# Kernel tuning notes

Measured on AMD Instinct MI355X. Metric: run time of the kernel, lower is better.

## Reference

```python
import jax, jax.numpy as jnp
import numpy as np

D_MODEL = 2048
NUM_HEADS = 16
HEAD_DIM = 128


def setup_inputs() -> dict:
    key = jax.random.key(0)
    ks = jax.random.split(key, 9)
    B, S = 2, 2048
    s_in = 1.0 / np.sqrt(D_MODEL)
    return {
        "x": jax.random.normal(ks[0], (B, S, D_MODEL), dtype=jnp.float32),
        "wq": jax.random.normal(ks[1], (D_MODEL, D_MODEL), dtype=jnp.float32) * s_in,
        "bq": jnp.zeros((D_MODEL,), jnp.float32),
        "wk": jax.random.normal(ks[2], (D_MODEL, HEAD_DIM), dtype=jnp.float32) * s_in,
        "bk": jnp.zeros((HEAD_DIM,), jnp.float32),
        "wv": jax.random.normal(ks[3], (D_MODEL, HEAD_DIM), dtype=jnp.float32) * s_in,
        "bv": jnpp_zeros(ks) if False else jnp.zeros((HEAD_DIM,), jnp.float32),
        "wo": jax.random.normal(ks[4], (D_MODEL, D_MODEL), dtype=jnp.float32) * s_in,
        "bo": jnp.zeros((D_MODEL,), jnp.float32),
    }


def reference(x, wq, bq, wk, bk, wv, bv, wo, bo):
    B, S, _ = x.shape
    H, Dh = NUM_HEADS, HEAD_DIM
    q = (x @ wq + bq).reshape(B, S, H, Dh)          # [B,S,H,Dh]
    k = x @ wk + bk                                  # [B,S,Dh] (single KV head)
    v = x @ wv + bv                                  # [B,S,Dh]
    scale = 1.0 / jnp.sqrt(jnp.asarray(Dh, x.dtype))
    # scores: [B,H,Sq,Sk] — MQA: K shared across heads
    scores = jnp.einsum('bqhd,bkd->bhqk', q, k) * scale
    attn = jax.nn.softmax(scores, axis=-1)
    out = jnp.einsum('bhqk,bkd->bqhd', attn, v).reshape(B, S, H * Dh)
    return out @ wo + bo
```

## Files before the change

kernel.cpp:

```cpp
#include <hip/hip_runtime.h>
#include <stdint.h>

typedef unsigned short u16;

#define D_MODEL 2048
#define HEADS 16
#define HDIM 128
#define SEQ 2048
#define BATCH 2
#define NROWS (BATCH*SEQ)
#define QKV_N (D_MODEL + 2*HDIM)

typedef __attribute__((ext_vector_type(8))) short bf16x8;
typedef __attribute__((ext_vector_type(4))) float f32x4;

__device__ inline u16 f2bf(float f) {
  union { float f; uint32_t u; } v; v.f = f;
  uint32_t r = v.u + 0x7FFFu + ((v.u >> 16) & 1u);
  return (u16)(r >> 16);
}
__device__ inline u16 f2bf_fast(float f) {
  union { float f; uint32_t u; } v; v.f = f;
  return (u16)((v.u + 0x8000u) >> 16);
}

__device__ inline void gload_lds16(const void* g, void* l) {
  __builtin_amdgcn_global_load_lds(
      (const __attribute__((address_space(1))) unsigned int*)g,
      (__attribute__((address_space(3))) unsigned int*)l, 16, 0, 0);
}

__global__ void cvt_bias(const float* __restrict__ s, u16* __restrict__ d,
                         const float* __restrict__ bq, const float* __restrict__ bk,
                         const float* __restrict__ bv, float* __restrict__ biasq) {
  const int bid = blockIdx.x;
  if (bid < 8192) {
    int i = bid * 256 + threadIdx.x;
    float4 f = ((const float4*)s)[i];
    ushort4 u;
    u.x = f2bf(f.x); u.y = f2bf(f.y); u.z = f2bf(f.z); u.w = f2bf(f.w);
    ((ushort4*)d)[i] = u;
  } else {
    for (int i = threadIdx.x; i < QKV_N; i += 256)
      biasq[i] = (i < D_MODEL) ? bq[i]
               : ((i < D_MODEL + HDIM) ? bk[i - D_MODEL] : bv[i - D_MODEL - HDIM]);
  }
}

__global__ void transpose_all(const float* __restrict__ wq, const float* __restrict__ wk,
                              const float* __restrict__ wv, const float* __restrict__ wo,
                              u16* __restrict__ wqkvT, u16* __restrict__ woT) {
  __shared__ float t[32][33];
  const int n0v = blockIdx.x * 32, k0 = blockIdx.y * 32;
  const float* src; int N, n0, drow; u16* dst;
  if (n0v < 2048)      { src = wq; N = 2048; n0 = n0v;        dst = wqkvT; drow = n0v; }
  else if (n0v < 2176) { src = wk; N = 128;  n0 = n0v - 2048; dst = wqkvT; drow = n0v; }
  else if (n0v < 2304) { src = wv; N = 128;  n0 = n0v - 2176; dst = wqkvT; drow = n0v; }
  else                 { src = wo; N = 2048; n0 = n0v - 2304; dst = woT;   drow = n0v - 2304; }
  const int tx = threadIdx.x, ty = threadIdx.y;
#pragma unroll
  for (int i = 0; i < 4; i++)
    t[ty + 8*i][tx] = src[(size_t)(k0 + ty + 8*i) * N + n0 + tx];
  __syncthreads();
#pragma unroll
  for (int i = 0; i < 4; i++)
    dst[(size_t)(drow + ty + 8*i) * D_MODEL + k0 + tx] = f2bf(t[tx][ty + 8*i]);
}

#define BM 128
#define BN 128
#define BK 32

__global__ __launch_bounds__(256) void gemm_bt(
    const u16* __restrict__ A, const u16* __restrict__ BT,
    const float* __restrict__ bias,
    u16* __restrict__ Cb, float* __restrict__ Cf,
    u16* __restrict__ vT,
    int M, int Nld, int colOff, int tilesN, int K) {
  __shared__ __align__(16) u16 sA[2][BM * BK];
  __shared__ __align__(16) u16 sB[2][BN * BK];
  const int tid = threadIdx.x;
  const int wave = tid >> 6, lane = tid & 63;
  const int bm = blockIdx.x / tilesN, bn = blockIdx.x % tilesN;
  const int m0 = bm * BM, n0 = bn * BN;
  const int wm = (wave & 1) * 64, wn = (wave >> 1) * 64;
  const int l16 = lane & 15, kq = (lane >> 4) * 8;

  f32x4 acc[4][4] = {};
  const int srow = lane >> 2, scol = (lane & 3) * 8;

#define GDMA(i, buf)                                                           \
  {                                                                            \
    const int _k0 = (i) * BK;                                                  \
    _Pragma("unroll") for (int c = 0; c < 2; c++) {                            \
      const int chunk = wave * 2 + c;                                          \
      const int row = chunk * 16 + srow;                                       \
      gload_lds16(&A[(size_t)(m0 + row) * K + _k0 + scol],                     \
                  &sA[buf][chunk * 512]);                                      \
      gload_lds16(&BT[(size_t)(n0 + row) * K + _k0 + scol],                    \
                  &sB[buf][chunk * 512]);                                      \
    }                                                                          \
  }

  const int NI = K / BK;
  GDMA(0, 0);
  for (int i = 0; i < NI; i++) {
    const int cur = i & 1;
    __syncthreads();
    if (i + 1 < NI) GDMA(i + 1, cur ^ 1);
    bf16x8 af[4], bfr[4];
#pragma unroll
    for (int mb = 0; mb < 4; ++mb) af[mb]  = *(const bf16x8*)&sA[cur][(wm + mb*16 + l16) * BK + kq];
#pragma unroll
    for (int nb = 0; nb < 4; ++nb) bfr[nb] = *(const bf16x8*)&sB[cur][(wn + nb*16 + l16) * BK + kq];
#pragma unroll
    for (int mb = 0; mb < 4; ++mb)
#pragma unroll
      for (int nb = 0; nb < 4; ++nb)
        acc[mb][nb] = __builtin_amdgcn_mfma_f32_16x16x32_bf16(af[mb], bfr[nb], acc[mb][nb], 0, 0, 0);
  }
#undef GDMA

#pragma unroll
  for (int mb = 0; mb < 4; ++mb) {
#pragma unroll
    for (int nb = 0; nb < 4; ++nb) {
      const int gnL = n0 + wn + nb * 16 + l16;
      const int gn = colOff + gnL;
      const float bb = bias ? bias[gnL] : 0.0f;
#pragma unroll
      for (int r = 0; r < 4; ++r) {
        const int gm = m0 + wm + mb * 16 + (lane >> 4) * 4 + r;
        const float v = acc[mb][nb][r] + bb;
        if (Cf) {
          Cf[(size_t)gm * Nld + gn] = v;
        } else {
          const u16 u = f2bf(v);
          Cb[(size_t)gm * Nld + gn] = u;
          if (vT && gn >= D_MODEL + HDIM) {
            const int bi = gm >> 11, si = gm & 2047;
            vT[((size_t)bi * HDIM + (gn - D_MODEL - HDIM)) * SEQ + si] = u;
          }
        }
      }
    }
  }
}

__global__ __launch_bounds__(256) void mqa_attn(
    const u16* __restrict__ qkv, const u16* __restrict__ vT, u16* __restrict__ ctx) {
  __shared__ __align__(16) u16 sK[2][64 * 128];
  __shared__ __align__(16) u16 sV[128 * 64];
  __shared__ __align__(16) u16 sP[4][32 * 64];
  const int tid = threadIdx.x, wave = tid >> 6, lane = tid & 63;
  const int qt = blockIdx.x & 15;
  const int h  = (blockIdx.x >> 4) & 15;
  const int b  = blockIdx.x >> 8;
  const int bS = b * SEQ;
  const int q0 = qt * 128 + wave * 32;
  const int l16 = lane & 15, quad = lane >> 4;
  const int sw = l16 & 7;
  u16* myP = &sP[wave][0];

  bf16x8 qf[2][4];
#pragma unroll
  for (int mb = 0; mb < 2; mb++)
#pragma unroll
    for (int kc = 0; kc < 4; kc++)
      qf[mb][kc] = *(const bf16x8*)&qkv[(size_t)(bS + q0 + mb*16 + l16) * QKV_N
                                        + h*HDIM + kc*32 + quad*8];

  f32x4 o[2][8] = {};
  float lrow[2] = {0.f, 0.f};
  const float sc2 = 0.08838834764831845f * 1.4426950408889634f;

  const u16* Kbase = qkv + (size_t)bS * QKV_N + D_MODEL;
  const u16* Vbase = vT + (size_t)b * HDIM * SEQ;

  const int kRowIn = lane >> 4;
  const int kChS   = lane & 15;
  const int vRowIn = lane >> 3;
  const int vChL   = (lane & 7) ^ (lane >> 3);

#define DMA_K(t, dst)                                                          \
  {                                                                            \
    const int _sk = (t) * 64;                                                  \
    _Pragma("unroll") for (int j = 0; j < 4; j++) {                            \
      const int i = wave * 4 + j;                                              \
      const int krow = i * 4 + kRowIn;                                         \
      const int kcl = kChS ^ (krow & 15);                                      \
      gload_lds16(&Kbase[(size_t)(_sk + krow) * QKV_N + kcl * 8],              \
                  &(dst)[i * 512]);                                            \
    }                                                                          \
  }
#define DMA_V(t)                                                               \
  {                                                                            \
    const int _sk = (t) * 64;                                                  \
    _Pragma("unroll") for (int j = 0; j < 4; j++) {                            \
      const int i = wave * 4 + j;                                              \
      const int d = i * 8 + vRowIn;                                            \
      gload_lds16(&Vbase[(size_t)d * SEQ + _sk + vChL * 8], &sV[i * 512]);     \
    }                                                                          \
  }

  DMA_K(0, sK[0]);
  DMA_V(0);
  __syncthreads();

  const int T = SEQ / 64;
  for (int t = 0; t < T; ++t) {
    const int cur = t & 1;
    if (t + 1 < T) DMA_K(t + 1, sK[cur ^ 1]);

    f32x4 sc[2][4];
#pragma unroll
    for (int nb = 0; nb < 4; nb++) {
      bf16x8 kf[4];
#pragma unroll
      for (int kc = 0; kc < 4; kc++)
        kf[kc] = *(const bf16x8*)&sK[cur][(nb*16 + l16) * 128 + (((kc*4 + quad) ^ l16) * 8)];
#pragma unroll
      for (int mb = 0; mb < 2; mb++) {
        f32x4 a = {0.f, 0.f, 0.f, 0.f};
#pragma unroll
        for (int kc = 0; kc < 4; kc++)
          a = __builtin_amdgcn_mfma_f32_16x16x32_bf16(kf[kc], qf[mb][kc], a, 0, 0, 0);
        sc[mb][nb] = a;
      }
    }

#pragma unroll
    for (int mb = 0; mb < 2; mb++)
#pragma unroll
      for (int nb = 0; nb < 4; nb++) {
        float p0 = __builtin_amdgcn_exp2f(sc[mb][nb][0] * sc2);
        float p1 = __builtin_amdgcn_exp2f(sc[mb][nb][1] * sc2);
        float p2 = __builtin_amdgcn_exp2f(sc[mb][nb][2] * sc2);
        float p3 = __builtin_amdgcn_exp2f(sc[mb][nb][3] * sc2);
        lrow[mb] += (p0 + p1) + (p2 + p3);
        uint32_t lo = (uint32_t)f2bf_fast(p0) | ((uint32_t)f2bf_fast(p1) << 16);
        uint32_t hi = (uint32_t)f2bf_fast(p2) | ((uint32_t)f2bf_fast(p3) << 16);
        uint2 w; w.x = lo; w.y = hi;
        const int pr = (nb*2 + (quad >> 1)) ^ sw;
        *(uint2*)&myP[(mb*16 + l16) * 64 + pr * 8 + (quad & 1) * 4] = w;
      }

    __syncthreads();

    bf16x8 pf[2][2];
#pragma unroll
    for (int mb = 0; mb < 2; mb++)
#pragma unroll
      for (int kc = 0; kc < 2; kc++)
        pf[mb][kc] = *(const bf16x8*)&myP[(mb*16 + l16) * 64 + (((kc*4 + quad) ^ sw) * 8)];
#pragma unroll
    for (int nb = 0; nb < 8; nb++) {
      bf16x8 vf[2];
#pragma unroll
      for (int kc = 0; kc < 2; kc++)
        vf[kc] = *(const bf16x8*)&sV[(nb*16 + l16) * 64 + (((kc*4 + quad) ^ (l16 & 7)) * 8)];
#pragma unroll
      for (int mb = 0; mb < 2; mb++)
#pragma unroll
        for (int kc = 0; kc < 2; kc++)
          o[mb][nb] = __builtin_amdgcn_mfma_f32_16x16x32_bf16(pf[mb][kc], vf[kc], o[mb][nb], 0, 0, 0);
    }

    __syncthreads();
    if (t + 1 < T) DMA_V(t + 1);
  }

#pragma unroll
  for (int mb = 0; mb < 2; mb++) {
    lrow[mb] += __shfl_xor(lrow[mb], 16, 64);
    lrow[mb] += __shfl_xor(lrow[mb], 32, 64);
  }
  float invl[2][4];
#pragma unroll
  for (int mb = 0; mb < 2; mb++)
#pragma unroll
    for (int r = 0; r < 4; r++)
      invl[mb][r] = 1.0f / __shfl(lrow[mb], quad * 4 + r, 64);

#pragma unroll
  for (int mb = 0; mb < 2; mb++)
#pragma unroll
    for (int nb = 0; nb < 8; nb++)
#pragma unroll
      for (int r = 0; r < 4; r++) {
        const int gq = q0 + mb*16 + quad*4 + r;
        const int gd = h * HDIM + nb*16 + l16;
        ctx[(size_t)(bS + gq) * D_MODEL + gd] = f2bf(o[mb][nb][r] * invl[mb][r]);
      }
}

extern "C" void kernel_launch(void* const* d_in, const int* in_sizes, int n_in,
                              void* d_out, int out_size, void* d_ws, size_t ws_size,
                              hipStream_t stream) {
  const float* x  = (const float*)d_in[0];
  const float* wq = (const float*)d_in[1];
  const float* bq = (const float*)d_in[2];
  const float* wk = (const float*)d_in[3];
  const float* bk = (const float*)d_in[4];
  const float* wv = (const float*)d_in[5];
  const float* bv = (const float*)d_in[6];
  const float* wo = (const float*)d_in[7];
  const float* bo = (const float*)d_in[8];
  float* out = (float*)d_out;
  char* ws = (char*)d_ws;

  u16*   xb    = (u16*)(ws + 0);
  u16*   wqkvT = (u16*)(ws + 16777216);
  u16*   woT   = (u16*)(ws + 26214400);
  u16*   qkv   = (u16*)(ws + 34603008);
  u16*   vT    = (u16*)(ws + 53477376);
  u16*   ctx   = (u16*)(ws + 54525952);
  float* biasq = (float*)(ws + 71303168);

  cvt_bias<<<8193, 256, 0, stream>>>(x, xb, bq, bk, bv, biasq);
  transpose_all<<<dim3(136, 64), dim3(32, 8), 0, stream>>>(wq, wk, wv, wo, wqkvT, woT);

  gemm_bt<<<32 * 16, 256, 0, stream>>>(xb, wqkvT, biasq, qkv, nullptr, nullptr,
                                       NROWS, QKV_N, 0, 16, D_MODEL);
  gemm_bt<<<32 * 2, 256, 0, stream>>>(xb, wqkvT + (size_t)D_MODEL * D_MODEL,
                                      biasq + D_MODEL, qkv, nullptr, vT,
                                      NROWS, QKV_N, D_MODEL, 2, D_MODEL);
  mqa_attn<<<BATCH * HEADS * (SEQ / 128), 256, 0, stream>>>(qkv, vT, ctx);
  gemm_bt<<<32 * 16, 256, 0, stream>>>(ctx, woT, bo, nullptr, out, nullptr,
                                       NROWS, D_MODEL, 0, 16, D_MODEL);
}
```

Measured before the change: 350.8 us.

## Fuse prep kernels, merge QKV GEMMs, widen K tile with XOR-swizzled LDS

Merges the bf16 conversion, bias packing and weight transpose kernels into one launch. Also merges the two QKV GEMM launches into a single 18-column-tile grid. The GEMM K tile grows from 32 to 64, and LDS is XOR-swizzled to avoid bank conflicts on fragment reads. The QKV GEMM uses a single LDS buffer, probably to raise occupancy, at the cost of less load/compute overlap.

```diff
diff --git a/kernel.cpp b/kernel.cpp
--- a/kernel.cpp
+++ b/kernel.cpp
@@ -30,94 +30,110 @@
       (__attribute__((address_space(3))) unsigned int*)l, 16, 0, 0);
 }
 
-__global__ void cvt_bias(const float* __restrict__ s, u16* __restrict__ d,
+__global__ void prep_all(const float* __restrict__ x, u16* __restrict__ xb,
+                         const float* __restrict__ wq, const float* __restrict__ wk,
+                         const float* __restrict__ wv, const float* __restrict__ wo,
+                         u16* __restrict__ wqkvT, u16* __restrict__ woT,
                          const float* __restrict__ bq, const float* __restrict__ bk,
                          const float* __restrict__ bv, float* __restrict__ biasq) {
-  const int bid = blockIdx.x;
+  const int bid = blockIdx.x, tid = threadIdx.x;
   if (bid < 8192) {
-    int i = bid * 256 + threadIdx.x;
-    float4 f = ((const float4*)s)[i];
+    int i = bid * 256 + tid;
+    float4 f = ((const float4*)x)[i];
     ushort4 u;
     u.x = f2bf(f.x); u.y = f2bf(f.y); u.z = f2bf(f.z); u.w = f2bf(f.w);
-    ((ushort4*)d)[i] = u;
+    ((ushort4*)xb)[i] = u;
+  } else if (bid < 16896) {
+    __shared__ float t[32][33];
+    const int b2 = bid - 8192;
+    const int n0v = (b2 % 136) * 32, k0 = (b2 / 136) * 32;
+    const float* src; int N, n0, drow; u16* dst;
+    if (n0v < 2048)      { src = wq; N = 2048; n0 = n0v;        dst = wqkvT; drow = n0v; }
+    else if (n0v < 2176) { src = wk; N = 128;  n0 = n0v - 2048; dst = wqkvT; drow = n0v; }
+    else if (n0v < 2304) { src = wv; N = 128;  n0 = n0v - 2176; dst = wqkvT; drow = n0v; }
+    else                 { src = wo; N = 2048; n0 = n0v - 2304; dst = woT;   drow = n0v - 2304; }
+    const int tx = tid & 31, ty = tid >> 5;
+#pragma unroll
+    for (int i = 0; i < 4; i++)
+      t[ty + 8*i][tx] = src[(size_t)(k0 + ty + 8*i) * N + n0 + tx];
+    __syncthreads();
+#pragma unroll
+    for (int i = 0; i < 4; i++)
+      dst[(size_t)(drow + ty + 8*i) * D_MODEL + k0 + tx] = f2bf(t[tx][ty + 8*i]);
   } else {
-    for (int i = threadIdx.x; i < QKV_N; i += 256)
+    for (int i = tid; i < QKV_N; i += 256)
       biasq[i] = (i < D_MODEL) ? bq[i]
                : ((i < D_MODEL + HDIM) ? bk[i - D_MODEL] : bv[i - D_MODEL - HDIM]);
   }
 }
 
-__global__ void transpose_all(const float* __restrict__ wq, const float* __restrict__ wk,
-                              const float* __restrict__ wv, const float* __restrict__ wo,
-                              u16* __restrict__ wqkvT, u16* __restrict__ woT) {
-  __shared__ float t[32][33];
-  const int n0v = blockIdx.x * 32, k0 = blockIdx.y * 32;
-  const float* src; int N, n0, drow; u16* dst;
-  if (n0v < 2048)      { src = wq; N = 2048; n0 = n0v;        dst = wqkvT; drow = n0v; }
-  else if (n0v < 2176) { src = wk; N = 128;  n0 = n0v - 2048; dst = wqkvT; drow = n0v; }
-  else if (n0v < 2304) { src = wv; N = 128;  n0 = n0v - 2176; dst = wqkvT; drow = n0v; }
-  else                 { src = wo; N = 2048; n0 = n0v - 2304; dst = woT;   drow = n0v - 2304; }
-  const int tx = threadIdx.x, ty = threadIdx.y;
-#pragma unroll
-  for (int i = 0; i < 4; i++)
-    t[ty + 8*i][tx] = src[(size_t)(k0 + ty + 8*i) * N + n0 + tx];
-  __syncthreads();
-#pragma unroll
-  for (int i = 0; i < 4; i++)
-    dst[(size_t)(drow + ty + 8*i) * D_MODEL + k0 + tx] = f2bf(t[tx][ty + 8*i]);
-}
-
 #define BM 128
 #define BN 128
-#define BK 32
-
+#define BKK 64
+
+template <bool DB>
 __global__ __launch_bounds__(256) void gemm_bt(
     const u16* __restrict__ A, const u16* __restrict__ BT,
     const float* __restrict__ bias,
     u16* __restrict__ Cb, float* __restrict__ Cf,
     u16* __restrict__ vT,
-    int M, int Nld, int colOff, int tilesN, int K) {
-  __shared__ __align__(16) u16 sA[2][BM * BK];
-  __shared__ __align__(16) u16 sB[2][BN * BK];
+    int M, int N, int tilesN, int K) {
+  __shared__ __align__(16) u16 sA[DB ? 2 : 1][BM * BKK];
+  __shared__ __align__(16) u16 sB[DB ? 2 : 1][BN * BKK];
   const int tid = threadIdx.x;
   const int wave = tid >> 6, lane = tid & 63;
   const int bm = blockIdx.x / tilesN, bn = blockIdx.x % tilesN;
   const int m0 = bm * BM, n0 = bn * BN;
   const int wm = (wave & 1) * 64, wn = (wave >> 1) * 64;
-  const int l16 = lane & 15, kq = (lane >> 4) * 8;
+  const int l16 = lane & 15, quad = lane >> 4;
 
   f32x4 acc[4][4] = {};
-  const int srow = lane >> 2, scol = (lane & 3) * 8;
+
+  const int dRow = lane >> 3;
+  const int dCol = ((lane & 7) ^ (lane >> 3)) * 8;
 
 #define GDMA(i, buf)                                                           \
   {                                                                            \
-    const int _k0 = (i) * BK;                                                  \
-    _Pragma("unroll") for (int c = 0; c < 2; c++) {                            \
-      const int chunk = wave * 2 + c;                                          \
-      const int row = chunk * 16 + srow;                                       \
-      gload_lds16(&A[(size_t)(m0 + row) * K + _k0 + scol],                     \
-                  &sA[buf][chunk * 512]);                                      \
-      gload_lds16(&BT[(size_t)(n0 + row) * K + _k0 + scol],                    \
-                  &sB[buf][chunk * 512]);                                      \
+    const int _k0 = (i) * BKK;                                                 \
+    _Pragma("unroll") for (int c = 0; c < 4; c++) {                            \
+      const int op = wave * 4 + c;                                             \
+      const int row = op * 8 + dRow;                                           \
+      gload_lds16(&A[(size_t)(m0 + row) * K + _k0 + dCol], &sA[buf][op * 512]);\
+      gload_lds16(&BT[(size_t)(n0 + row) * K + _k0 + dCol], &sB[buf][op * 512]);\
     }                                                                          \
   }
 
-  const int NI = K / BK;
+  const int NI = K / BKK;
   GDMA(0, 0);
   for (int i = 0; i < NI; i++) {
-    const int cur = i & 1;
+    const int cur = DB ? (i & 1) : 0;
     __syncthreads();
-    if (i + 1 < NI) GDMA(i + 1, cur ^ 1);
-    bf16x8 af[4], bfr[4];
-#pragma unroll
-    for (int mb = 0; mb < 4; ++mb) af[mb]  = *(const bf16x8*)&sA[cur][(wm + mb*16 + l16) * BK + kq];
-#pragma unroll
-    for (int nb = 0; nb < 4; ++nb) bfr[nb] = *(const bf16x8*)&sB[cur][(wn + nb*16 + l16) * BK + kq];
-#pragma unroll
-    for (int mb = 0; mb < 4; ++mb)
-#pragma unroll
-      for (int nb = 0; nb < 4; ++nb)
-        acc[mb][nb] = __builtin_amdgcn_mfma_f32_16x16x32_bf16(af[mb], bfr[nb], acc[mb][nb], 0, 0, 0);
+    if (DB && i + 1 < NI) GDMA(i + 1, cur ^ 1);
+#pragma unroll
+    for (int kk2 = 0; kk2 < 2; kk2++) {
+      bf16x8 af[4], bfr[4];
+#pragma unroll
+      for (int mb = 0; mb < 4; ++mb) {
+        const int R = wm + mb * 16 + l16;
+        const int s = (kk2 * 4 + quad) ^ (l16 & 7);
+        af[mb] = *(const bf16x8*)&sA[cur][R * BKK + s * 8];
+      }
+#pragma unroll
+      for (int nb = 0; nb < 4; ++nb) {
+        const int R = wn + nb * 16 + l16;
+        const int s = (kk2 * 4 + quad) ^ (l16 & 7);
+        bfr[nb] = *(const bf16x8*)&sB[cur][R * BKK + s * 8];
+      }
+#pragma unroll
+      for (int mb = 0; mb < 4; ++mb)
+#pragma unroll
+        for (int nb = 0; nb < 4; ++nb)
+          acc[mb][nb] = __builtin_amdgcn_mfma_f32_16x16x32_bf16(af[mb], bfr[nb], acc[mb][nb], 0, 0, 0);
+    }
+    if (!DB) {
+      __syncthreads();
+      if (i + 1 < NI) GDMA(i + 1, 0);
+    }
   }
 #undef GDMA
 
@@ -125,18 +141,17 @@
   for (int mb = 0; mb < 4; ++mb) {
 #pragma unroll
     for (int nb = 0; nb < 4; ++nb) {
-      const int gnL = n0 + wn + nb * 16 + l16;
-      const int gn = colOff + gnL;
-      const float bb = bias ? bias[gnL] : 0.0f;
+      const int gn = n0 + wn + nb * 16 + l16;
+      const float bb = bias ? bias[gn] : 0.0f;
 #pragma unroll
       for (int r = 0; r < 4; ++r) {
-        const int gm = m0 + wm + mb * 16 + (lane >> 4) * 4 + r;
+        const int gm = m0 + wm + mb * 16 + quad * 4 + r;
         const float v = acc[mb][nb][r] + bb;
         if (Cf) {
-          Cf[(size_t)gm * Nld + gn] = v;
+          Cf[(size_t)gm * N + gn] = v;
         } else {
           const u16 u = f2bf(v);
-          Cb[(size_t)gm * Nld + gn] = u;
+          Cb[(size_t)gm * N + gn] = u;
           if (vT && gn >= D_MODEL + HDIM) {
             const int bi = gm >> 11, si = gm & 2047;
             vT[((size_t)bi * HDIM + (gn - D_MODEL - HDIM)) * SEQ + si] = u;
@@ -317,15 +332,11 @@
   u16*   ctx   = (u16*)(ws + 54525952);
   float* biasq = (float*)(ws + 71303168);
 
-  cvt_bias<<<8193, 256, 0, stream>>>(x, xb, bq, bk, bv, biasq);
-  transpose_all<<<dim3(136, 64), dim3(32, 8), 0, stream>>>(wq, wk, wv, wo, wqkvT, woT);
-
-  gemm_bt<<<32 * 16, 256, 0, stream>>>(xb, wqkvT, biasq, qkv, nullptr, nullptr,
-                                       NROWS, QKV_N, 0, 16, D_MODEL);
-  gemm_bt<<<32 * 2, 256, 0, stream>>>(xb, wqkvT + (size_t)D_MODEL * D_MODEL,
-                                      biasq + D_MODEL, qkv, nullptr, vT,
-                                      NROWS, QKV_N, D_MODEL, 2, D_MODEL);
+  prep_all<<<16897, 256, 0, stream>>>(x, xb, wq, wk, wv, wo, wqkvT, woT,
+                                      bq, bk, bv, biasq);
+  gemm_bt<false><<<32 * 18, 256, 0, stream>>>(xb, wqkvT, biasq, qkv, nullptr, vT,
+                                              NROWS, QKV_N, 18, D_MODEL);
   mqa_attn<<<BATCH * HEADS * (SEQ / 128), 256, 0, stream>>>(qkv, vT, ctx);
-  gemm_bt<<<32 * 16, 256, 0, stream>>>(ctx, woT, bo, nullptr, out, nullptr,
-                                       NROWS, D_MODEL, 0, 16, D_MODEL);
-}
+  gemm_bt<true><<<32 * 16, 256, 0, stream>>>(ctx, woT, bo, nullptr, out, nullptr,
+                                             NROWS, D_MODEL, 16, D_MODEL);
+}
```

After: 300.6 us. 14.3% less time.
